# Kernel optimization log

Measured on AMD Instinct MI355X. Metric: run time of the kernel, lower is better.

Reference implementation:

```python
import jax, jax.numpy as jnp
import numpy as np

DIM = 1536
NH = 12
HD = DIM // NH          # 128
C = HD // 2             # 64 complex freq slots per head
DT = C - 2 * (C // 3)   # 22 temporal
DS = C // 3             # 21 per spatial axis
EPS = 1e-6
M_TAB = 64              # rope table length (>= max(f,h,w))


def _rope_tables():
    def tab(d):
        inv = 1.0 / (10000.0 ** (np.arange(d, dtype=np.float64) / d))
        ang = np.outer(np.arange(M_TAB, dtype=np.float64), inv)
        return np.cos(ang), np.sin(ang)
    ct, st = tab(DT)
    ch, sh = tab(DS)
    cw, sw = tab(DS)
    fc = np.concatenate([ct, ch, cw], axis=1).astype(np.float32)  # [M, 64]
    fs = np.concatenate([st, sh, sw], axis=1).astype(np.float32)
    return jnp.asarray(fc), jnp.asarray(fs)


def setup_inputs() -> dict:
    key = jax.random.key(0)
    ks = jax.random.split(key, 6)
    B, F, H, W = 1, 8, 22, 40
    L = F * H * W  # 7040
    s = 0.02
    x = jax.random.normal(ks[0], (B, L, DIM), jnp.float32)
    Wq = jax.random.normal(ks[1], (DIM, DIM), jnp.float32) * s
    Wk = jax.random.normal(ks[2], (DIM, DIM), jnp.float32) * s
    Wv = jax.random.normal(ks[3], (DIM, DIM), jnp.float32) * s
    Wo = jax.random.normal(ks[4], (DIM, DIM), jnp.float32) * s
    bk2 = jax.random.split(ks[5], 4)
    bq = jax.random.normal(bk2[0], (DIM,), jnp.float32) * s
    bk = jax.random.normal(bk2[1], (DIM,), jnp.float32) * s
    bv = jax.random.normal(bk2[2], (DIM,), jnp.float32) * s
    bo = jax.random.normal(bk2[3], (DIM,), jnp.float32) * s
    fc, fs = _rope_tables()
    return dict(x=x, Wq=Wq, bq=bq, Wk=Wk, bk=bk, Wv=Wv, bv=bv, Wo=Wo, bo=bo,
                gq=jnp.ones((DIM,), jnp.float32), gk=jnp.ones((DIM,), jnp.float32),
                freqs_cos=fc, freqs_sin=fs,
                num_frames=F, grid_h=H, grid_w=W,
                chunk_size=2, sink_size=1, max_attention_size=2640)


def _pos_table(tab, f, h, w):
    # tab: [M, 64] -> per-token [f*h*w, 64] via (t,h,w) axis split [22,21,21]
    t = jnp.broadcast_to(tab[:f, :DT][:, None, None, :], (f, h, w, DT))
    hh = jnp.broadcast_to(tab[:h, DT:DT + DS][None, :, None, :], (f, h, w, DS))
    ww = jnp.broadcast_to(tab[:w, DT + DS:][None, None, :, :], (f, h, w, DS))
    return jnp.concatenate([t, hh, ww], axis=-1).reshape(f * h * w, C)


def _forward(x, Wq, bq, Wk, bk, Wv, bv, Wo, bo, gq, gk, freqs_cos, freqs_sin,
             num_frames, grid_h, grid_w, chunk_size, sink_size, max_attention_size):
    B, L, D = x.shape
    lin = lambda t, W, b: jnp.einsum('bld,ed->ble', t, W) + b
    rms = lambda t, g: t * jax.lax.rsqrt(jnp.mean(t * t, axis=-1, keepdims=True) + EPS) * g

    q = rms(lin(x, Wq, bq), gq).reshape(B, L, NH, HD)
    k = rms(lin(x, Wk, bk), gk).reshape(B, L, NH, HD)
    v = lin(x, Wv, bv).reshape(B, L, NH, HD)

    # causal RoPE (start_frame=0)
    cosL = _pos_table(freqs_cos, num_frames, grid_h, grid_w)  # [L, 64]
    sinL = _pos_table(freqs_sin, num_frames, grid_h, grid_w)

    def rope(t):
        a = t.reshape(B, L, NH, C, 2)
        xr, xi = a[..., 0], a[..., 1]
        co = cosL[None, :, None, :]
        si = sinL[None, :, None, :]
        return jnp.stack([xr * co - xi * si, xr * si + xi * co], axis=-1).reshape(B, L, NH, HD)

    q = rope(q)
    k = rope(k)

    # loop attention, diffusion forcing: chunk i attends [0,(i+1)*block) with sink+window
    frame_seqlen = grid_h * grid_w
    block = frame_seqlen * chunk_size
    total_len = num_frames * frame_seqlen
    sink_end = sink_size * frame_seqlen
    num_chunks = -(-total_len // block)
    scale = 1.0 / (HD ** 0.5)

    def attn(qi, ki, vi):
        s = jnp.einsum('bqnd,bknd->bnqk', qi, ki) * scale
        p = jax.nn.softmax(s, axis=-1)
        return jnp.einsum('bnqk,bknd->bqnd', p, vi)

    outs = []
    for i in range(num_chunks):
        q_start = i * block
        q_end = min((i + 1) * block, total_len)
        qi = q[:, q_start:q_end]
        chunk_end = q_end
        if max_attention_size == -1 or sink_end == 0:
            if max_attention_size == -1:
                ki, vi = k[:, :chunk_end], v[:, :chunk_end]
            else:
                ws = max(0, chunk_end - max_attention_size)
                ki, vi = k[:, ws:chunk_end], v[:, ws:chunk_end]
        else:
            window = max_attention_size - sink_end
            ws = max(sink_end, chunk_end - window)
            ki = jnp.concatenate([k[:, :sink_end], k[:, ws:chunk_end]], axis=1)
            vi = jnp.concatenate([v[:, :sink_end], v[:, ws:chunk_end]], axis=1)
        outs.append(attn(qi, ki, vi))

    o = jnp.concatenate(outs, axis=1).reshape(B, L, D)
    return jnp.einsum('bld,ed->ble', o, Wo) + bo


def reference(x, Wq, bq, Wk, bk, Wv, bv, Wo, bo, gq, gk, freqs_cos, freqs_sin,
              num_frames, grid_h, grid_w, chunk_size, sink_size, max_attention_size):
    return _forward(x, Wq, bq, Wk, bk, Wv, bv, Wo, bo, gq, gk, freqs_cos, freqs_sin,
                    num_frames, grid_h, grid_w, chunk_size, sink_size, max_attention_size)
```

## Files before the change

kernel.cpp:

```cpp
#include <hip/hip_runtime.h>
#include <math.h>

typedef __attribute__((ext_vector_type(8))) short short8;
typedef __attribute__((ext_vector_type(4))) float f32x4;
typedef __attribute__((ext_vector_type(16))) float f32x16;
typedef __attribute__((ext_vector_type(4))) float f4;
typedef __attribute__((ext_vector_type(4))) unsigned short us4;
typedef __attribute__((ext_vector_type(2))) unsigned int u32x2;

#define MFMA16(a,b,c) __builtin_amdgcn_mfma_f32_16x16x32_bf16(a,b,c,0,0,0)
#define MFMA32(a,b,c) __builtin_amdgcn_mfma_f32_32x32x16_bf16(a,b,c,0,0,0)

__device__ __forceinline__ unsigned short f2bf(float f) {
  unsigned int u = __float_as_uint(f);
  u = (u + 0x7FFFu + ((u >> 16) & 1u)) >> 16;
  return (unsigned short)u;
}
__device__ __forceinline__ float bf2f(unsigned short b) {
  return __uint_as_float(((unsigned int)b) << 16);
}
__device__ __forceinline__ unsigned int pk2(float a, float b) {
  unsigned int au = __float_as_uint(a) + 0x8000u;
  unsigned int bu = __float_as_uint(b) + 0x8000u;
  return __builtin_amdgcn_perm(bu, au, 0x07060302u);
}

typedef const __attribute__((address_space(1))) unsigned int* gas_t;
typedef __attribute__((address_space(3))) unsigned int* las_t;
__device__ __forceinline__ void gl16(const void* g, void* l) {
  __builtin_amdgcn_global_load_lds((gas_t)g, (las_t)l, 16, 0, 0);
}

__global__ void cvt_f32_bf16(const float* __restrict__ in,
                             unsigned short* __restrict__ out, int n4) {
  int i = blockIdx.x * blockDim.x + threadIdx.x;
  const int stride = gridDim.x * blockDim.x;
  for (; i < n4; i += stride) {
    f4 v = ((const f4*)in)[i];
    us4 o;
    o[0] = f2bf(v[0]); o[1] = f2bf(v[1]); o[2] = f2bf(v[2]); o[3] = f2bf(v[3]);
    ((us4*)out)[i] = o;
  }
}

__global__ __launch_bounds__(256)
void vtrans(const unsigned short* __restrict__ qkv, unsigned short* __restrict__ vt)
{
  __shared__ unsigned int tile[64][65];
  const int lb = blockIdx.x * 64;
  const int rb = blockIdx.y * 64;
  const int tid = threadIdx.x;

#pragma unroll
  for (int i = 0; i < 2; ++i) {
    int task = i * 256 + tid;
    int l = task >> 3, c = task & 7;
    short8 v = *(const short8*)(qkv + (long)(lb + l) * 4608 + 3072 + rb + c * 8);
#pragma unroll
    for (int e = 0; e < 8; ++e) tile[c * 8 + e][l] = (unsigned short)v[e];
  }
  __syncthreads();
#pragma unroll
  for (int i = 0; i < 2; ++i) {
    int task = i * 256 + tid;
    int r = task >> 3, c = task & 7;
    short8 o;
#pragma unroll
    for (int e = 0; e < 8; ++e) o[e] = (short)tile[r][c * 8 + e];
    *(short8*)(vt + (long)(rb + r) * 7040 + lb + c * 8) = o;
  }
}

template<int F32OUT>
__global__ __launch_bounds__(256)
void gemm_bt(const unsigned short* __restrict__ A,
             const unsigned short* __restrict__ B,
             const float* __restrict__ bias,
             unsigned short* __restrict__ obf,
             float* __restrict__ of32,
             int K, int ldo)
{
  const int tid = threadIdx.x;
  const int wave = tid >> 6, lane = tid & 63, lg = lane >> 4, lr = lane & 15;
  const int wr = wave >> 1, wc = wave & 1;
  const int m0 = blockIdx.y * 128, n0 = blockIdx.x * 128;

  __shared__ __align__(16) unsigned short Al[128 * 32];
  __shared__ __align__(16) unsigned short Bl[128 * 32];

  f32x4 acc[4][4];
#pragma unroll
  for (int m = 0; m < 4; ++m)
#pragma unroll
    for (int n = 0; n < 4; ++n) acc[m][n] = (f32x4){0.f, 0.f, 0.f, 0.f};

  const int r0 = tid >> 2, r1 = (tid + 256) >> 2;
  const int c0 = (tid & 3) * 8;
  const long arow0 = (long)(m0 + r0) * K, arow1 = (long)(m0 + r1) * K;
  const long brow0 = (long)(n0 + r0) * K, brow1 = (long)(n0 + r1) * K;

  for (int k0 = 0; k0 < K; k0 += 32) {
    gl16(A + arow0 + k0 + c0, (char*)Al + tid * 16);
    gl16(A + arow1 + k0 + c0, (char*)Al + (tid + 256) * 16);
    gl16(B + brow0 + k0 + c0, (char*)Bl + tid * 16);
    gl16(B + brow1 + k0 + c0, (char*)Bl + (tid + 256) * 16);
    __syncthreads();
    short8 af[4], bf[4];
#pragma unroll
    for (int m = 0; m < 4; ++m)
      af[m] = *(const short8*)(Al + (wr * 64 + m * 16 + lr) * 32 + lg * 8);
#pragma unroll
    for (int n = 0; n < 4; ++n)
      bf[n] = *(const short8*)(Bl + (wc * 64 + n * 16 + lr) * 32 + lg * 8);
#pragma unroll
    for (int m = 0; m < 4; ++m)
#pragma unroll
      for (int n = 0; n < 4; ++n)
        acc[m][n] = MFMA16(af[m], bf[n], acc[m][n]);
    __syncthreads();
  }

#pragma unroll
  for (int n = 0; n < 4; ++n) {
    const int col = n0 + wc * 64 + n * 16 + lr;
    const float bs = bias[col];
#pragma unroll
    for (int m = 0; m < 4; ++m) {
      const int row = m0 + wr * 64 + m * 16 + lg * 4;
#pragma unroll
      for (int r = 0; r < 4; ++r) {
        float v = acc[m][n][r] + bs;
        if (F32OUT) of32[(long)(row + r) * ldo + col] = v;
        else        obf[(long)(row + r) * ldo + col] = f2bf(v);
      }
    }
  }
}

__global__ __launch_bounds__(256)
void normrope(unsigned short* __restrict__ qkv, const float* __restrict__ g,
              const float* __restrict__ fc, const float* __restrict__ fs,
              int colOff, float oscale)
{
  const int l = blockIdx.x, tid = threadIdx.x;
  __shared__ float rowbuf[1536];
  __shared__ float sred[4];
  unsigned short* rp = qkv + (long)l * 4608 + colOff;

  float ss = 0.f;
  if (tid < 192) {
    short8 v = *(const short8*)(rp + tid * 8);
#pragma unroll
    for (int e = 0; e < 8; ++e) {
      float f = bf2f((unsigned short)v[e]);
      rowbuf[tid * 8 + e] = f;
      ss += f * f;
    }
  }
#pragma unroll
  for (int m = 32; m; m >>= 1) ss += __shfl_xor(ss, m, 64);
  if ((tid & 63) == 0) sred[tid >> 6] = ss;
  __syncthreads();
  const float rs = rsqrtf((sred[0] + sred[1] + sred[2] + sred[3]) * (1.f / 1536.f) + 1e-6f);

  const int f_ = l / 880, rem = l % 880, h_ = rem / 40, w_ = rem % 40;
#pragma unroll
  for (int j = 0; j < 3; ++j) {
    int p = tid + j * 256;
    int head = p >> 6, c = p & 63;
    int e = head * 128 + 2 * c;
    int tr = (c < 22) ? f_ : ((c < 43) ? h_ : w_);
    float co = fc[tr * 64 + c], si = fs[tr * 64 + c];
    float xr = rowbuf[e] * rs * g[e];
    float xi = rowbuf[e + 1] * rs * g[e + 1];
    float yr = (xr * co - xi * si) * oscale;
    float yi = (xr * si + xi * co) * oscale;
    unsigned int pk = (unsigned int)f2bf(yr) | ((unsigned int)f2bf(yi) << 16);
    *(unsigned int*)(rp + e) = pk;
  }
}

__device__ __forceinline__ void issueK(const unsigned short* __restrict__ qkv,
                                       int h, int t, int kvlen, int woff, int tid,
                                       unsigned short* Kbuf)
{
#pragma unroll
  for (int i = 0; i < 4; ++i) {
    int s = i * 256 + tid;
    int kvl = s >> 4;
    int dc = (s & 15) ^ (kvl & 7);
    int j = t * 64 + kvl; j = j < kvlen ? j : kvlen - 1;
    int gk = j + (j >= 880 ? woff : 0);
    gl16(qkv + (long)gk * 4608 + 1536 + h * 128 + dc * 8, (char*)Kbuf + s * 16);
  }
}

__device__ __forceinline__ void issueV(const unsigned short* __restrict__ vt,
                                       int h, int t, int kvlen, int woff, int tid,
                                       unsigned short* Vbuf)
{
#pragma unroll
  for (int i = 0; i < 4; ++i) {
    int s = i * 256 + tid;
    int d = s >> 3;
    int c = (s & 7) ^ (d & 7);
    int j = t * 64 + c * 8;
    j = j < kvlen ? j : kvlen - 8;
    int gk = j + (j >= 880 ? woff : 0);
    gl16(vt + (long)(h * 128 + d) * 7040 + gk, (char*)Vbuf + s * 16);
  }
}

__global__ __launch_bounds__(256, 2)
void attn_kern(const unsigned short* __restrict__ qkv,
               const unsigned short* __restrict__ vt,
               unsigned short* __restrict__ ob)
{
  const int qt = blockIdx.x, ci = blockIdx.y, h = blockIdx.z;
  const int tid = threadIdx.x, wave = tid >> 6, lane = tid & 63;
  const int l31 = lane & 31, hh = lane >> 5;
  const int chunk_start = ci * 1760, chunk_end = chunk_start + 1760;
  const int wstart = (ci == 0) ? 880 : ci * 1760;
  const int woff = wstart - 880;
  const int kvlen = 880 + (chunk_end - wstart);
  const int q0 = chunk_start + qt * 128;

  __shared__ __align__(16) unsigned short Kl[2][64 * 128];
  __shared__ __align__(16) unsigned short Vt[2][128 * 64];

  int qr = q0 + wave * 32 + l31;
  if (qr >= chunk_end) qr = chunk_end - 1;
  const unsigned short* qp = qkv + (long)qr * 4608 + h * 128;
  short8 qf[8];
#pragma unroll
  for (int st = 0; st < 8; ++st) qf[st] = *(const short8*)(qp + st * 16 + hh * 8);

  f32x16 Oc[4];
#pragma unroll
  for (int i = 0; i < 4; ++i)
#pragma unroll
    for (int j = 0; j < 16; ++j) Oc[i][j] = 0.f;
  float m_run = -1e30f, l_run = 0.f;
  unsigned int w0[8], w1[8];

  auto computeQK = [&](int t, int cur, f32x16* S0, f32x16* S1) {
    f32x16 a0, a1;
#pragma unroll
    for (int j = 0; j < 16; ++j) { a0[j] = 0.f; a1[j] = 0.f; }
    __builtin_amdgcn_s_setprio(1);
#pragma unroll
    for (int st = 0; st < 8; ++st) {
      int off = 32 * st + 16 * hh;
      int b0 = l31 * 256 + (off ^ ((l31 & 7) << 4));
      short8 k0 = *(const short8*)((const char*)&Kl[cur][0] + b0);
      a0 = MFMA32(k0, qf[st], a0);
      int b1 = (32 + l31) * 256 + (off ^ ((l31 & 7) << 4));
      short8 k1 = *(const short8*)((const char*)&Kl[cur][0] + b1);
      a1 = MFMA32(k1, qf[st], a1);
    }
    __builtin_amdgcn_s_setprio(0);
    if (t * 64 + 64 > kvlen) {
#pragma unroll
      for (int r = 0; r < 16; ++r) {
        int kv0 = t * 64 + (r & 3) + 8 * (r >> 2) + 4 * hh;
        if (kv0 >= kvlen)      a0[r] = -1e30f;
        if (kv0 + 32 >= kvlen) a1[r] = -1e30f;
      }
    }
    *S0 = a0; *S1 = a1;
  };

  auto finishTile = [&](f32x16& s0f, f32x16& s1f) {
    float mx[16];
#pragma unroll
    for (int r = 0; r < 16; ++r) mx[r] = fmaxf(s0f[r], s1f[r]);
#pragma unroll
    for (int w = 8; w; w >>= 1)
#pragma unroll
      for (int r = 0; r < w; ++r) mx[r] = fmaxf(mx[r], mx[r + w]);
    float pm = fmaxf(mx[0], __shfl_xor(mx[0], 32, 64));
    const bool defer = __all(pm <= m_run + 8.f);
    const float mn = defer ? m_run : fmaxf(m_run, pm);
#pragma unroll
    for (int r = 0; r < 16; ++r) {
      s0f[r] = __builtin_amdgcn_exp2f(s0f[r] - mn);
      s1f[r] = __builtin_amdgcn_exp2f(s1f[r] - mn);
    }
    float sm[16];
#pragma unroll
    for (int r = 0; r < 16; ++r) sm[r] = s0f[r] + s1f[r];
#pragma unroll
    for (int w = 8; w; w >>= 1)
#pragma unroll
      for (int r = 0; r < w; ++r) sm[r] += sm[r + w];
    float sum = sm[0] + __shfl_xor(sm[0], 32, 64);
    if (defer) {
      l_run += sum;
    } else {
      float al = __builtin_amdgcn_exp2f(m_run - mn);
      l_run = l_run * al + sum;
      m_run = mn;
#pragma unroll
      for (int i = 0; i < 4; ++i)
#pragma unroll
        for (int j = 0; j < 16; ++j) Oc[i][j] *= al;
    }
#pragma unroll
    for (int m = 0; m < 8; ++m) {
      w0[m] = pk2(s0f[2 * m], s0f[2 * m + 1]);
      w1[m] = pk2(s1f[2 * m], s1f[2 * m + 1]);
    }
  };

  auto doPV = [&](int cur) {
    __builtin_amdgcn_s_setprio(1);
#pragma unroll
    for (int s = 0; s < 4; ++s) {
      const unsigned int* w = (s < 2) ? w0 : w1;
      const int lo4 = (s & 1) * 4;
      unsigned int x0 = __shfl_xor(w[lo4 + 2], 32, 64);
      unsigned int x1 = __shfl_xor(w[lo4 + 3], 32, 64);
      unsigned int y0 = __shfl_xor(w[lo4],     32, 64);
      unsigned int y1 = __shfl_xor(w[lo4 + 1], 32, 64);
      unsigned int fw[4];
      fw[0] = hh ? x0 : w[lo4];
      fw[1] = hh ? x1 : w[lo4 + 1];
      fw[2] = hh ? w[lo4 + 2] : y0;
      fw[3] = hh ? w[lo4 + 3] : y1;
      short8 pb = *(const short8*)fw;
#pragma unroll
      for (int dt = 0; dt < 4; ++dt) {
        int d = dt * 32 + l31;
        int byte = (d * 128 + s * 32 + hh * 16) ^ ((d & 7) << 4);
        short8 vf = *(const short8*)((const char*)&Vt[cur][0] + byte);
        Oc[dt] = MFMA32(vf, pb, Oc[dt]);
      }
    }
    __builtin_amdgcn_s_setprio(0);
  };

  const int nt = (kvlen + 63) >> 6;

  issueK(qkv, h, 0, kvlen, woff, tid, &Kl[0][0]);
  if (nt > 1) issueK(qkv, h, 1, kvlen, woff, tid, &Kl[1][0]);
  issueV(vt, h, 0, kvlen, woff, tid, &Vt[0][0]);
  __syncthreads();

  f32x16 sp0, sp1;
  computeQK(0, 0, &sp0, &sp1);
  __syncthreads();

  for (int t = 0; t < nt - 1; ++t) {
    const int cur = t & 1;
    if (t + 2 < nt) issueK(qkv, h, t + 2, kvlen, woff, tid, &Kl[cur][0]);
    issueV(vt, h, t + 1, kvlen, woff, tid, &Vt[cur ^ 1][0]);

    f32x16 sc0, sc1;
    computeQK(t + 1, cur ^ 1, &sc0, &sc1);
    finishTile(sp0, sp1);
    doPV(cur);
    __syncthreads();
    sp0 = sc0; sp1 = sc1;
  }
  finishTile(sp0, sp1);
  doPV((nt - 1) & 1);

  const int qg = q0 + wave * 32 + l31;
  if (qg < chunk_end) {
    const float inv = 1.f / l_run;
    unsigned short* op = ob + (long)qg * 1536 + h * 128;
#pragma unroll
    for (int dt = 0; dt < 4; ++dt) {
#pragma unroll
      for (int gblk = 0; gblk < 4; ++gblk) {
        int d = dt * 32 + gblk * 8 + hh * 4;
        unsigned int u0 = pk2(Oc[dt][4 * gblk]     * inv, Oc[dt][4 * gblk + 1] * inv);
        unsigned int u1 = pk2(Oc[dt][4 * gblk + 2] * inv, Oc[dt][4 * gblk + 3] * inv);
        u32x2 uu; uu[0] = u0; uu[1] = u1;
        *(u32x2*)(op + d) = uu;
      }
    }
  }
}

extern "C" void kernel_launch(void* const* d_in, const int* in_sizes, int n_in,
                              void* d_out, int out_size, void* d_ws, size_t ws_size,
                              hipStream_t stream)
{
  const float* x  = (const float*)d_in[0];
  const float* Wq = (const float*)d_in[1];
  const float* bq = (const float*)d_in[2];
  const float* Wk = (const float*)d_in[3];
  const float* bk = (const float*)d_in[4];
  const float* Wv = (const float*)d_in[5];
  const float* bv = (const float*)d_in[6];
  const float* Wo = (const float*)d_in[7];
  const float* bo = (const float*)d_in[8];
  const float* gq = (const float*)d_in[9];
  const float* gk = (const float*)d_in[10];
  const float* fc = (const float*)d_in[11];
  const float* fs = (const float*)d_in[12];

  char* ws = (char*)d_ws;
  unsigned short* xb   = (unsigned short*)(ws);
  unsigned short* wcat = (unsigned short*)(ws + 21626880);
  unsigned short* wob  = (unsigned short*)(ws + 35782656);
  float*          bcat = (float*)(ws + 40501248);
  unsigned short* qkv  = (unsigned short*)(ws + 40519680);
  unsigned short* obuf = (unsigned short*)(ws + 105400320);
  unsigned short* vtb  = xb;

  cvt_f32_bf16<<<2048, 256, 0, stream>>>(x,  xb,   10813440 / 4);
  cvt_f32_bf16<<<1024, 256, 0, stream>>>(Wq, wcat,            2359296 / 4);
  cvt_f32_bf16<<<1024, 256, 0, stream>>>(Wk, wcat + 2359296,  2359296 / 4);
  cvt_f32_bf16<<<1024, 256, 0, stream>>>(Wv, wcat + 4718592,  2359296 / 4);
  cvt_f32_bf16<<<1024, 256, 0, stream>>>(Wo, wob,             2359296 / 4);
  hipMemcpyAsync(bcat,        bq, 1536 * 4, hipMemcpyDeviceToDevice, stream);
  hipMemcpyAsync(bcat + 1536, bk, 1536 * 4, hipMemcpyDeviceToDevice, stream);
  hipMemcpyAsync(bcat + 3072, bv, 1536 * 4, hipMemcpyDeviceToDevice, stream);

  gemm_bt<0><<<dim3(36, 55), 256, 0, stream>>>(xb, wcat, bcat, qkv, nullptr, 1536, 4608);

  vtrans<<<dim3(110, 24), 256, 0, stream>>>(qkv, vtb);

  const float qsc = (float)(1.4426950408889634 / sqrt(128.0));
  normrope<<<7040, 256, 0, stream>>>(qkv, gq, fc, fs, 0,    qsc);
  normrope<<<7040, 256, 0, stream>>>(qkv, gk, fc, fs, 1536, 1.0f);

  attn_kern<<<dim3(14, 4, 12), 256, 0, stream>>>(qkv, vtb, obuf);

  gemm_bt<1><<<dim3(12, 55), 256, 0, stream>>>(obuf, wob, bo, nullptr, (float*)d_out, 1536, 1536);
}
```

Measured before the change: 454.6 us.

## Single-buffer V tile, raise attention occupancy, reorder blocks heavy-chunk-first

The attention kernel drops V from double to single buffering in shared memory, which cuts LDS per block so launch bounds can allow three blocks per CU. The V tile is now loaded after the PV step, and explicit vmcnt waits plus raw barriers replace __syncthreads so the K and V tiles are waited on separately. The grid is flattened so chunks 1-3, which have the longer KV windows, are scheduled before chunk 0. Tradeoffs: V loads are less overlapped with compute, the kernel has more barriers, and the tighter register budget for three blocks per CU may cause spills.

```diff
diff --git a/kernel.cpp b/kernel.cpp
--- a/kernel.cpp
+++ b/kernel.cpp
@@ -29,6 +29,14 @@
 typedef __attribute__((address_space(3))) unsigned int* las_t;
 __device__ __forceinline__ void gl16(const void* g, void* l) {
   __builtin_amdgcn_global_load_lds((gas_t)g, (las_t)l, 16, 0, 0);
+}
+
+__device__ __forceinline__ void vm_wait8() { asm volatile("s_waitcnt vmcnt(8)" ::: "memory"); }
+__device__ __forceinline__ void vm_wait4() { asm volatile("s_waitcnt vmcnt(4)" ::: "memory"); }
+__device__ __forceinline__ void vm_wait0() { asm volatile("s_waitcnt vmcnt(0)" ::: "memory"); }
+__device__ __forceinline__ void barrier_fence() {
+  __builtin_amdgcn_s_barrier();
+  __builtin_amdgcn_sched_barrier(0);
 }
 
 __global__ void cvt_f32_bf16(const float* __restrict__ in,
@@ -211,12 +219,16 @@
   }
 }
 
-__global__ __launch_bounds__(256, 2)
+__global__ __launch_bounds__(256, 3)
 void attn_kern(const unsigned short* __restrict__ qkv,
                const unsigned short* __restrict__ vt,
                unsigned short* __restrict__ ob)
 {
-  const int qt = blockIdx.x, ci = blockIdx.y, h = blockIdx.z;
+  int bi = blockIdx.x, ci, rem;
+  if (bi < 504) { ci = 1 + bi / 168; rem = bi % 168; }
+  else          { ci = 0;            rem = bi - 504; }
+  const int h = rem / 14, qt = rem % 14;
+
   const int tid = threadIdx.x, wave = tid >> 6, lane = tid & 63;
   const int l31 = lane & 31, hh = lane >> 5;
   const int chunk_start = ci * 1760, chunk_end = chunk_start + 1760;
@@ -226,7 +238,7 @@
   const int q0 = chunk_start + qt * 128;
 
   __shared__ __align__(16) unsigned short Kl[2][64 * 128];
-  __shared__ __align__(16) unsigned short Vt[2][128 * 64];
+  __shared__ __align__(16) unsigned short Vt[128 * 64];
 
   int qr = q0 + wave * 32 + l31;
   if (qr >= chunk_end) qr = chunk_end - 1;
@@ -312,7 +324,7 @@
     }
   };
 
-  auto doPV = [&](int cur) {
+  auto doPV = [&]() {
     __builtin_amdgcn_s_setprio(1);
 #pragma unroll
     for (int s = 0; s < 4; ++s) {
@@ -332,7 +344,7 @@
       for (int dt = 0; dt < 4; ++dt) {
         int d = dt * 32 + l31;
         int byte = (d * 128 + s * 32 + hh * 16) ^ ((d & 7) << 4);
-        short8 vf = *(const short8*)((const char*)&Vt[cur][0] + byte);
+        short8 vf = *(const short8*)((const char*)&Vt[0] + byte);
         Oc[dt] = MFMA32(vf, pb, Oc[dt]);
       }
     }
@@ -342,28 +354,40 @@
   const int nt = (kvlen + 63) >> 6;
 
   issueK(qkv, h, 0, kvlen, woff, tid, &Kl[0][0]);
-  if (nt > 1) issueK(qkv, h, 1, kvlen, woff, tid, &Kl[1][0]);
-  issueV(vt, h, 0, kvlen, woff, tid, &Vt[0][0]);
-  __syncthreads();
+  issueK(qkv, h, 1, kvlen, woff, tid, &Kl[1][0]);
+  issueV(vt, h, 0, kvlen, woff, tid, &Vt[0]);
+  vm_wait8();
+  barrier_fence();
 
   f32x16 sp0, sp1;
   computeQK(0, 0, &sp0, &sp1);
-  __syncthreads();
+  barrier_fence();
 
   for (int t = 0; t < nt - 1; ++t) {
     const int cur = t & 1;
-    if (t + 2 < nt) issueK(qkv, h, t + 2, kvlen, woff, tid, &Kl[cur][0]);
-    issueV(vt, h, t + 1, kvlen, woff, tid, &Vt[cur ^ 1][0]);
+    const bool pf2 = (t + 2 < nt);
+    if (pf2) issueK(qkv, h, t + 2, kvlen, woff, tid, &Kl[cur][0]);
+
+    if (pf2) vm_wait8(); else vm_wait4();
+    barrier_fence();
 
     f32x16 sc0, sc1;
     computeQK(t + 1, cur ^ 1, &sc0, &sc1);
     finishTile(sp0, sp1);
-    doPV(cur);
-    __syncthreads();
+
+    if (pf2) vm_wait4(); else vm_wait0();
+    barrier_fence();
+
+    doPV();
+    barrier_fence();
+    issueV(vt, h, t + 1, kvlen, woff, tid, &Vt[0]);
     sp0 = sc0; sp1 = sc1;
   }
+
+  vm_wait0();
+  barrier_fence();
   finishTile(sp0, sp1);
-  doPV((nt - 1) & 1);
+  doPV();
 
   const int qg = q0 + wave * 32 + l31;
   if (qg < chunk_end) {
@@ -427,7 +451,7 @@
   normrope<<<7040, 256, 0, stream>>>(qkv, gq, fc, fs, 0,    qsc);
   normrope<<<7040, 256, 0, stream>>>(qkv, gk, fc, fs, 1536, 1.0f);
 
-  attn_kern<<<dim3(14, 4, 12), 256, 0, stream>>>(qkv, vtb, obuf);
+  attn_kern<<<672, 256, 0, stream>>>(qkv, vtb, obuf);
 
   gemm_bt<1><<<dim3(12, 55), 256, 0, stream>>>(obuf, wob, bo, nullptr, (float*)d_out, 1536, 1536);
 }
```

After: 814.6 us. +79.2%, slower.
